# Performance work log

Measured on AMD Instinct MI355X. Metric: run time of the kernel, lower is better.

The kernel has to match this reference:

```python
import jax, jax.numpy as jnp
import numpy as np
import math

SCALES = [1, 2, 4, 8]
H = 1024           # hidden_size
NS = len(SCALES)
DS = H // NS       # per-scale dim = 256
NH_S = max(1, 8 // NS)  # heads per scale = 2


def _avg_pool(x, s):
    # x: [B, L, d], kernel=stride=s (L divisible by s)
    B, L, d = x.shape
    return x.reshape(B, L // s, s, d).mean(axis=2)


def _mha(q, k, v, in_w, in_b, out_w, out_b, nh):
    # torch nn.MultiheadAttention, batch_first, no mask.
    d = q.shape[-1]
    wq, wk, wv = in_w[:d], in_w[d:2 * d], in_w[2 * d:]
    bq, bk, bv = in_b[:d], in_b[d:2 * d], in_b[2 * d:]
    qh = q @ wq.T + bq
    kh = k @ wk.T + bk
    vh = v @ wv.T + bv
    B, Lq, _ = qh.shape
    Lk = kh.shape[1]
    hd = d // nh
    qh = qh.reshape(B, Lq, nh, hd).transpose(0, 2, 1, 3)
    kh = kh.reshape(B, Lk, nh, hd).transpose(0, 2, 1, 3)
    vh = vh.reshape(B, Lk, nh, hd).transpose(0, 2, 1, 3)
    scores = jnp.einsum('bhqd,bhkd->bhqk', qh, kh) * (1.0 / math.sqrt(hd))
    w = jax.nn.softmax(scores, axis=-1)
    out = jnp.einsum('bhqk,bhkd->bhqd', w, vh)
    out = out.transpose(0, 2, 1, 3).reshape(B, Lq, d)
    out = out @ out_w.T + out_b
    return out, w.mean(axis=1)  # averaged attn weights (torch default)


def setup_inputs() -> dict:
    key = jax.random.key(0)
    ks = jax.random.split(key, 20)
    B, S = 4, 2048
    f = lambda k, shape: (jax.random.normal(k, shape, dtype=jnp.float32) * 0.02)
    return {
        'query': jax.random.normal(ks[0], (B, S, H), dtype=jnp.float32),
        'key': jax.random.normal(ks[1], (B, S, H), dtype=jnp.float32),
        'value': jax.random.normal(ks[2], (B, S, H), dtype=jnp.float32),
        'wq': f(ks[3], (H, H)), 'bq': f(ks[4], (H,)),
        'wk': f(ks[5], (H, H)), 'bk': f(ks[6], (H,)),
        'wv': f(ks[7], (H, H)), 'bv': f(ks[8], (H,)),
        'mha_in_w': f(ks[9], (NS, 3 * DS, DS)),
        'mha_in_b': f(ks[10], (NS, 3 * DS)),
        'mha_out_w': f(ks[11], (NS, DS, DS)),
        'mha_out_b': f(ks[12], (NS, DS)),
        'fus_w': f(ks[13], (H, H)), 'fus_b': f(ks[14], (H,)),
    }


def reference(query, key, value, wq, bq, wk, bk, wv, bv,
              mha_in_w, mha_in_b, mha_out_w, mha_out_b, fus_w, fus_b):
    q = query @ wq.T + bq
    k = key @ wk.T + bk
    v = value @ wv.T + bv
    outs = []
    weights0 = None
    for i, s in enumerate(SCALES):
        qs = q[..., i * DS:(i + 1) * DS]
        ks_ = k[..., i * DS:(i + 1) * DS]
        vs = v[..., i * DS:(i + 1) * DS]
        if s > 1:
            ks_ = _avg_pool(ks_, s)
            vs = _avg_pool(vs, s)
        attended, w = _mha(qs, ks_, vs, mha_in_w[i], mha_in_b[i],
                           mha_out_w[i], mha_out_b[i], NH_S)
        # F.interpolate back to seq_len is an identity here (query length == seq_len)
        outs.append(attended)
        if i == 0:
            weights0 = w
    fused = jnp.concatenate(outs, axis=-1) @ fus_w.T + fus_b
    return fused, weights0
```

## Files before the change

kernel.cpp:

```cpp
#include <hip/hip_runtime.h>
#include <stdint.h>

typedef unsigned short u16;
typedef __bf16 v8bf __attribute__((ext_vector_type(8)));
typedef float v4f __attribute__((ext_vector_type(4)));
typedef __attribute__((address_space(3))) unsigned lds_t;
typedef const __attribute__((address_space(1))) unsigned g_t;

__device__ __forceinline__ u16 f2bf(float f) {
  union { float f; unsigned u; } v; v.f = f;
  unsigned r = v.u + 0x7FFFu + ((v.u >> 16) & 1u);
  return (u16)(r >> 16);
}
__device__ __forceinline__ float bf2f(u16 h) {
  union { unsigned u; float f; } v; v.u = ((unsigned)h) << 16;
  return v.f;
}
__device__ __forceinline__ ushort4 f4bf(float4 f) {
  ushort4 o;
  o.x = f2bf(f.x); o.y = f2bf(f.y); o.z = f2bf(f.z); o.w = f2bf(f.w);
  return o;
}
__device__ __forceinline__ long sel4(long4 v, int z) {
  return z == 0 ? v.x : z == 1 ? v.y : z == 2 ? v.z : v.w;
}
__device__ __forceinline__ int sel4i(int4 v, int z) {
  return z == 0 ? v.x : z == 1 ? v.y : z == 2 ? v.z : v.w;
}

__global__ void k_cvt(const float* __restrict__ s, u16* __restrict__ d, long n) {
  long i = ((long)blockIdx.x * blockDim.x + threadIdx.x) * 4;
  long stride = (long)gridDim.x * blockDim.x * 4;
  for (; i < n; i += stride) {
    *(ushort4*)(d + i) = f4bf(*(const float4*)(s + i));
  }
}

__global__ void k_cvtpool(const float* __restrict__ src, u16* __restrict__ dst) {
  int g = blockIdx.x & 255, b = blockIdx.x >> 8;
  int c = threadIdx.x * 4;
  const float* p = src + ((long)b * 2048 + g * 8) * 1024 + c;
  u16* df = dst + ((long)b * 2048 + g * 8) * 1024 + c;
  float4 x[8];
#pragma unroll
  for (int j = 0; j < 8; j++) {
    x[j] = *(const float4*)(p + (long)j * 1024);
    *(ushort4*)(df + (long)j * 1024) = f4bf(x[j]);
  }
  float4 s2[4], s4[2], s8;
#pragma unroll
  for (int j = 0; j < 4; j++) {
    s2[j].x = x[2 * j].x + x[2 * j + 1].x;
    s2[j].y = x[2 * j].y + x[2 * j + 1].y;
    s2[j].z = x[2 * j].z + x[2 * j + 1].z;
    s2[j].w = x[2 * j].w + x[2 * j + 1].w;
  }
#pragma unroll
  for (int j = 0; j < 2; j++) {
    s4[j].x = s2[2 * j].x + s2[2 * j + 1].x;
    s4[j].y = s2[2 * j].y + s2[2 * j + 1].y;
    s4[j].z = s2[2 * j].z + s2[2 * j + 1].z;
    s4[j].w = s2[2 * j].w + s2[2 * j + 1].w;
  }
  s8.x = s4[0].x + s4[1].x; s8.y = s4[0].y + s4[1].y;
  s8.z = s4[0].z + s4[1].z; s8.w = s4[0].w + s4[1].w;
  u16* d2 = dst + ((long)8192 + b * 1024 + g * 4) * 1024 + c;
#pragma unroll
  for (int j = 0; j < 4; j++) {
    float4 t = {s2[j].x * 0.5f, s2[j].y * 0.5f, s2[j].z * 0.5f, s2[j].w * 0.5f};
    *(ushort4*)(d2 + (long)j * 1024) = f4bf(t);
  }
  u16* d4 = dst + ((long)12288 + b * 512 + g * 2) * 1024 + c;
#pragma unroll
  for (int j = 0; j < 2; j++) {
    float4 t = {s4[j].x * 0.25f, s4[j].y * 0.25f, s4[j].z * 0.25f, s4[j].w * 0.25f};
    *(ushort4*)(d4 + (long)j * 1024) = f4bf(t);
  }
  float4 t8 = {s8.x * 0.125f, s8.y * 0.125f, s8.z * 0.125f, s8.w * 0.125f};
  *(ushort4*)(dst + ((long)14336 + b * 256 + g) * 1024 + c) = f4bf(t8);
}

__global__ void k_tc(const float* __restrict__ src, u16* __restrict__ dst, int R, int C) {
  __shared__ float t[32][33];
  long zoff = (long)blockIdx.z * R * C;
  int r0 = blockIdx.y * 32, c0 = blockIdx.x * 32;
  int tx = threadIdx.x & 31, ty = threadIdx.x >> 5;
#pragma unroll
  for (int j = 0; j < 32; j += 8)
    t[ty + j][tx] = src[zoff + (long)(r0 + ty + j) * C + c0 + tx];
  __syncthreads();
#pragma unroll
  for (int j = 0; j < 32; j += 8)
    dst[zoff + (long)(c0 + ty + j) * R + r0 + tx] = f2bf(t[tx][ty + j]);
}

__global__ void k_bcomb_qkv(const float* __restrict__ in_w, const float* __restrict__ in_b,
                            const float* __restrict__ bq, const float* __restrict__ bk,
                            const float* __restrict__ bv, float* __restrict__ out) {
  int gw = (blockIdx.x * 256 + threadIdx.x) >> 6;
  int lane = threadIdx.x & 63;
  int p = gw >> 10, j = gw & 1023, i = j >> 8, of = j & 255;
  const float* bp = p == 0 ? bq : p == 1 ? bk : bv;
  const float* row = in_w + ((long)i * 768 + p * 256 + of) * 256;
  float s = 0.f;
#pragma unroll
  for (int m = 0; m < 4; m++) s += row[lane + m * 64] * bp[i * 256 + lane + m * 64];
#pragma unroll
  for (int m = 32; m >= 1; m >>= 1) s += __shfl_xor(s, m, 64);
  if (lane == 0) out[gw] = in_b[(long)i * 768 + p * 256 + of] + s;
}

__global__ void k_bcomb_f(const float* __restrict__ fw, const float* __restrict__ fb,
                          const float* __restrict__ ob, float* __restrict__ out) {
  int w = (blockIdx.x * 256 + threadIdx.x) >> 6;
  int lane = threadIdx.x & 63;
  const float* row = fw + (long)w * 1024;
  float s = 0.f;
  for (int k = lane; k < 1024; k += 64) s += row[k] * ob[k];
#pragma unroll
  for (int m = 32; m >= 1; m >>= 1) s += __shfl_xor(s, m, 64);
  if (lane == 0) out[w] = fb[w] + s;
}

template<int KS>
__global__ __launch_bounds__(256) void k_ksum(const float* __restrict__ P,
                                              u16* __restrict__ O, long n, int coloff) {
  long i = ((long)blockIdx.x * 256 + threadIdx.x) * 4;
  if (i >= n) return;
  float4 s = *(const float4*)(P + i);
#pragma unroll
  for (int ks = 1; ks < KS; ks++) {
    float4 t = *(const float4*)(P + (long)ks * n + i);
    s.x += t.x; s.y += t.y; s.z += t.z; s.w += t.w;
  }
  *(ushort4*)(O + (i >> 8) * 1024 + coloff + (int)(i & 255)) = f4bf(s);
}

__device__ __forceinline__ float block_allreduce(float x, bool domax) {
  __shared__ float t[4];
  int lane = threadIdx.x & 63, w = threadIdx.x >> 6;
#pragma unroll
  for (int m = 32; m >= 1; m >>= 1) {
    float o = __shfl_xor(x, m, 64);
    x = domax ? fmaxf(x, o) : (x + o);
  }
  __syncthreads();
  if (lane == 0) t[w] = x;
  __syncthreads();
  return domax ? fmaxf(fmaxf(t[0], t[1]), fmaxf(t[2], t[3]))
               : (t[0] + t[1] + t[2] + t[3]);
}

__global__ __launch_bounds__(256) void k_softmax0(u16* __restrict__ P, float* __restrict__ W0) {
  int bq = blockIdx.x;
  int b = bq >> 11, q = bq & 2047;
  int tid = threadIdx.x;
  float pw[2][8];
  for (int h = 0; h < 2; h++) {
    u16* p = P + (((long)(b * 2 + h) * 2048 + q) * 2048);
    float v[8];
    float mx = -1e30f;
#pragma unroll
    for (int i = 0; i < 8; i++) { v[i] = bf2f(p[tid + i * 256]); mx = fmaxf(mx, v[i]); }
    mx = block_allreduce(mx, true);
    float s = 0.f;
#pragma unroll
    for (int i = 0; i < 8; i++) { v[i] = __expf(v[i] - mx); s += v[i]; }
    s = block_allreduce(s, false);
    float inv = 1.0f / s;
#pragma unroll
    for (int i = 0; i < 8; i++) { pw[h][i] = v[i] * inv; p[tid + i * 256] = f2bf(pw[h][i]); }
  }
  float* wrow = W0 + (long)bq * 2048;
#pragma unroll
  for (int i = 0; i < 8; i++) wrow[tid + i * 256] = 0.5f * (pw[0][i] + pw[1][i]);
}

__global__ __launch_bounds__(256) void k_flash(
    const u16* __restrict__ QHf, const u16* __restrict__ KH,
    const u16* __restrict__ VHT, u16* __restrict__ AOf)
{
  int z = blockIdx.z;
  int i = (z >> 3) + 1;
  int b = (z >> 1) & 3, h = z & 1;
  int Ls = 2048 >> i;
  int nkt = Ls >> 7;
  long ro = (long)(16384 - (8192 >> (i - 1))) * 256;
  int q0 = blockIdx.y * 64;

  __shared__ u16 QP[64][136];
  __shared__ u16 KV[2][128][32];
  __shared__ float red[2][4][64];

  const int tid = threadIdx.x, lane = tid & 63, wave = tid >> 6;
  const int q4 = lane >> 4, l16 = lane & 15;
  const int wr = (wave >> 1) * 32, wc = (wave & 1) * 64;
  const int srow = wave * 16 + (lane >> 2);
  const int scol = (lane & 3) * 8;

  {
    const u16* gq = QHf + ((long)b * 2048 + q0) * 1024 + i * 256 + h * 128;
    int idx = tid * 4;
#pragma unroll
    for (int j = 0; j < 4; j++) {
      int r = (idx + j) >> 4, ch = (idx + j) & 15;
      *(ulonglong2*)&QP[r][ch * 8] = *(const ulonglong2*)(gq + (long)r * 1024 + ch * 8);
    }
  }
  __syncthreads();
  v8bf qf[2][4];
#pragma unroll
  for (int mi = 0; mi < 2; mi++)
#pragma unroll
    for (int sub = 0; sub < 4; sub++)
      qf[mi][sub] = *(const v8bf*)&QP[wr + mi * 16 + l16][sub * 32 + q4 * 8];
  __syncthreads();

  const u16* gK = KH + ro + (long)b * Ls * 256 + h * 128;
  const u16* gV = VHT + ro + (long)(b * 2 + h) * 128 * Ls;

  auto stageK = [&](int buf, int kt, int sub) {
    const u16* g = gK + (long)(kt * 128 + srow) * 256 + sub * 32 + scol;
    __builtin_amdgcn_global_load_lds((g_t*)g, (lds_t*)&KV[buf][wave * 16][0], 16, 0, 0);
    __builtin_amdgcn_global_load_lds((g_t*)(g + 64 * 256), (lds_t*)&KV[buf][64 + wave * 16][0], 16, 0, 0);
  };
  auto stageV = [&](int buf, int kt, int sub) {
    const u16* g = gV + (long)srow * Ls + kt * 128 + sub * 32 + scol;
    __builtin_amdgcn_global_load_lds((g_t*)g, (lds_t*)&KV[buf][wave * 16][0], 16, 0, 0);
    __builtin_amdgcn_global_load_lds((g_t*)(g + (long)64 * Ls), (lds_t*)&KV[buf][64 + wave * 16][0], 16, 0, 0);
  };

  v4f acc_o[2][4];
  float m_run[2][4], l_run[2][4];
#pragma unroll
  for (int mi = 0; mi < 2; mi++)
#pragma unroll
    for (int ni = 0; ni < 4; ni++) acc_o[mi][ni] = (v4f){0.f, 0.f, 0.f, 0.f};
#pragma unroll
  for (int mi = 0; mi < 2; mi++)
#pragma unroll
    for (int i4 = 0; i4 < 4; i4++) { m_run[mi][i4] = -1e30f; l_run[mi][i4] = 0.f; }

  const float alpha = 0.08838834764831845f;

  for (int kt = 0; kt < nkt; kt++) {
    v4f s[2][4];
#pragma unroll
    for (int mi = 0; mi < 2; mi++)
#pragma unroll
      for (int ni = 0; ni < 4; ni++) s[mi][ni] = (v4f){0.f, 0.f, 0.f, 0.f};
    stageK(0, kt, 0);
    __syncthreads();
    int cur = 0;
#pragma unroll
    for (int sub = 0; sub < 4; sub++) {
      if (sub < 3) stageK(cur ^ 1, kt, sub + 1);
      v8bf kf[4];
#pragma unroll
      for (int ni = 0; ni < 4; ni++)
        kf[ni] = *(const v8bf*)&KV[cur][wc + ni * 16 + l16][q4 * 8];
#pragma unroll
      for (int mi = 0; mi < 2; mi++)
#pragma unroll
        for (int ni = 0; ni < 4; ni++)
          s[mi][ni] = __builtin_amdgcn_mfma_f32_16x16x32_bf16(qf[mi][sub], kf[ni], s[mi][ni], 0, 0, 0);
      __syncthreads();
      cur ^= 1;
    }
    stageV(0, kt, 0);

#pragma unroll
    for (int mi = 0; mi < 2; mi++)
#pragma unroll
      for (int ni = 0; ni < 4; ni++) s[mi][ni] *= alpha;
    float mloc[2][4];
#pragma unroll
    for (int mi = 0; mi < 2; mi++)
#pragma unroll
      for (int i4 = 0; i4 < 4; i4++)
        mloc[mi][i4] = fmaxf(fmaxf(s[mi][0][i4], s[mi][1][i4]),
                             fmaxf(s[mi][2][i4], s[mi][3][i4]));
#pragma unroll
    for (int d = 1; d <= 8; d <<= 1)
#pragma unroll
      for (int mi = 0; mi < 2; mi++)
#pragma unroll
        for (int i4 = 0; i4 < 4; i4++)
          mloc[mi][i4] = fmaxf(mloc[mi][i4], __shfl_xor(mloc[mi][i4], d, 64));
    if (l16 == 0) {
#pragma unroll
      for (int mi = 0; mi < 2; mi++)
#pragma unroll
        for (int i4 = 0; i4 < 4; i4++)
          red[0][wave][wr + mi * 16 + q4 * 4 + i4] = mloc[mi][i4];
    }
    __syncthreads();
    float scl[2][4];
#pragma unroll
    for (int mi = 0; mi < 2; mi++)
#pragma unroll
      for (int i4 = 0; i4 < 4; i4++) {
        int rr = wr + mi * 16 + q4 * 4 + i4;
        float mn = fmaxf(fmaxf(red[0][wave][rr], red[0][wave ^ 1][rr]), m_run[mi][i4]);
        scl[mi][i4] = __expf(m_run[mi][i4] - mn);
        m_run[mi][i4] = mn;
      }
    float lloc[2][4] = {{0.f, 0.f, 0.f, 0.f}, {0.f, 0.f, 0.f, 0.f}};
#pragma unroll
    for (int mi = 0; mi < 2; mi++)
#pragma unroll
      for (int ni = 0; ni < 4; ni++)
#pragma unroll
        for (int i4 = 0; i4 < 4; i4++) {
          float p = __expf(s[mi][ni][i4] - m_run[mi][i4]);
          lloc[mi][i4] += p;
          QP[wr + mi * 16 + q4 * 4 + i4][wc + ni * 16 + l16] = f2bf(p);
        }
#pragma unroll
    for (int d = 1; d <= 8; d <<= 1)
#pragma unroll
      for (int mi = 0; mi < 2; mi++)
#pragma unroll
        for (int i4 = 0; i4 < 4; i4++)
          lloc[mi][i4] += __shfl_xor(lloc[mi][i4], d, 64);
    if (l16 == 0) {
#pragma unroll
      for (int mi = 0; mi < 2; mi++)
#pragma unroll
        for (int i4 = 0; i4 < 4; i4++)
          red[1][wave][wr + mi * 16 + q4 * 4 + i4] = lloc[mi][i4];
    }
#pragma unroll
    for (int mi = 0; mi < 2; mi++)
#pragma unroll
      for (int ni = 0; ni < 4; ni++)
#pragma unroll
        for (int i4 = 0; i4 < 4; i4++) acc_o[mi][ni][i4] *= scl[mi][i4];
    __syncthreads();
#pragma unroll
    for (int mi = 0; mi < 2; mi++)
#pragma unroll
      for (int i4 = 0; i4 < 4; i4++) {
        int rr = wr + mi * 16 + q4 * 4 + i4;
        l_run[mi][i4] = l_run[mi][i4] * scl[mi][i4] + red[1][wave][rr] + red[1][wave ^ 1][rr];
      }

    int cv = 0;
#pragma unroll
    for (int sub = 0; sub < 4; sub++) {
      if (sub < 3) stageV(cv ^ 1, kt, sub + 1);
      v8bf pf[2], vf[4];
#pragma unroll
      for (int mi = 0; mi < 2; mi++)
        pf[mi] = *(const v8bf*)&QP[wr + mi * 16 + l16][sub * 32 + q4 * 8];
#pragma unroll
      for (int ni = 0; ni < 4; ni++)
        vf[ni] = *(const v8bf*)&KV[cv][wc + ni * 16 + l16][q4 * 8];
#pragma unroll
      for (int mi = 0; mi < 2; mi++)
#pragma unroll
        for (int ni = 0; ni < 4; ni++)
          acc_o[mi][ni] = __builtin_amdgcn_mfma_f32_16x16x32_bf16(pf[mi], vf[ni], acc_o[mi][ni], 0, 0, 0);
      __syncthreads();
      cv ^= 1;
    }
  }

#pragma unroll
  for (int mi = 0; mi < 2; mi++)
#pragma unroll
    for (int i4 = 0; i4 < 4; i4++) {
      float inv = 1.0f / l_run[mi][i4];
#pragma unroll
      for (int ni = 0; ni < 4; ni++) {
        int r = q0 + wr + mi * 16 + q4 * 4 + i4;
        int c = wc + ni * 16 + l16;
        AOf[((long)b * 2048 + r) * 1024 + i * 256 + h * 128 + c] =
            f2bf(acc_o[mi][ni][i4] * inv);
      }
    }
}

template<int WBF>
__global__ __launch_bounds__(256) void k_gemm(
    const u16* __restrict__ A, long ldA, long sA1, long sA2,
    const u16* __restrict__ B, long ldB, long sB1, long sB2,
    void* __restrict__ Cv, long ldC, long sC1, long sC2, long sCk,
    const float* __restrict__ bias, long sBias, float alpha,
    int M, int N, int K, int nz2, int KS)
{
  __shared__ u16 As[2][128][32];
  __shared__ u16 Bs[2][128][32];
  int z = blockIdx.z;
  int ks = z % KS; int zz = z / KS;
  int z1 = zz / nz2, z2 = zz - z1 * nz2;
  A += (long)z1 * sA1 + (long)z2 * sA2 + (long)ks * K;
  B += (long)z1 * sB1 + (long)z2 * sB2 + (long)ks * K;
  long coff = (long)z1 * sC1 + (long)z2 * sC2 + (long)ks * sCk;
  const float* bz = bias ? bias + (long)z2 * sBias : nullptr;
  const int m0 = blockIdx.y * 128, n0 = blockIdx.x * 128;
  const int tid = threadIdx.x;
  const int lane = tid & 63;
  const int wave = tid >> 6;
  const int wr = (wave >> 1) * 64, wc = (wave & 1) * 64;
  const int q4 = lane >> 4, l16 = lane & 15;

  const int srow = wave * 16 + (lane >> 2);
  const int scol = (lane & 3) * 8;
  const u16* gA = A + (long)(m0 + srow) * ldA + scol;
  const u16* gB = B + (long)(n0 + srow) * ldB + scol;

  auto stage = [&](int buf, int kt) {
    __builtin_amdgcn_global_load_lds((g_t*)(gA + kt), (lds_t*)&As[buf][wave * 16][0], 16, 0, 0);
    __builtin_amdgcn_global_load_lds((g_t*)(gA + 64 * ldA + kt), (lds_t*)&As[buf][64 + wave * 16][0], 16, 0, 0);
    __builtin_amdgcn_global_load_lds((g_t*)(gB + kt), (lds_t*)&Bs[buf][wave * 16][0], 16, 0, 0);
    __builtin_amdgcn_global_load_lds((g_t*)(gB + 64 * ldB + kt), (lds_t*)&Bs[buf][64 + wave * 16][0], 16, 0, 0);
  };

  v4f acc[4][4];
#pragma unroll
  for (int i = 0; i < 4; i++)
#pragma unroll
    for (int j = 0; j < 4; j++) acc[i][j] = (v4f){0.f, 0.f, 0.f, 0.f};

  stage(0, 0);
  __syncthreads();
  int cur = 0;
  for (int kt = 0; kt < K; kt += 32) {
    if (kt + 32 < K) stage(cur ^ 1, kt + 32);
    v8bf af[4], bf[4];
#pragma unroll
    for (int i = 0; i < 4; i++) af[i] = *(const v8bf*)&As[cur][wr + i * 16 + l16][q4 * 8];
#pragma unroll
    for (int i = 0; i < 4; i++) bf[i] = *(const v8bf*)&Bs[cur][wc + i * 16 + l16][q4 * 8];
#pragma unroll
    for (int mi = 0; mi < 4; mi++)
#pragma unroll
      for (int ni = 0; ni < 4; ni++)
        acc[mi][ni] = __builtin_amdgcn_mfma_f32_16x16x32_bf16(af[mi], bf[ni], acc[mi][ni], 0, 0, 0);
    __syncthreads();
    cur ^= 1;
  }

#pragma unroll
  for (int mi = 0; mi < 4; mi++) {
    int rb = m0 + wr + mi * 16 + q4 * 4;
#pragma unroll
    for (int ni = 0; ni < 4; ni++) {
      int c = n0 + wc + ni * 16 + l16;
      float bv = bz ? bz[c] : 0.f;
#pragma unroll
      for (int i = 0; i < 4; i++) {
        int r = rb + i;
        float val = acc[mi][ni][i] * alpha + bv;
        if (WBF) ((u16*)Cv)[coff + (long)r * ldC + c] = f2bf(val);
        else     ((float*)Cv)[coff + (long)r * ldC + c] = val;
      }
    }
  }
}

template<int TR>
__global__ __launch_bounds__(256) void k_gemm_sm(
    const u16* __restrict__ A, long ldA, long4 aOff,
    const u16* __restrict__ B, long ldB, long sB,
    u16* __restrict__ C, long ldC, long4 cOff,
    const float* __restrict__ bias, long sBias,
    int4 Mz, int K, int4 Lsz)
{
  int z = blockIdx.z;
  int M = sel4i(Mz, z);
  int m0 = blockIdx.y * 128;
  if (m0 >= M) return;
  int n0 = blockIdx.x * 64;
  const u16* Az = A + sel4(aOff, z);
  const u16* Bz = B + (long)z * sB;
  long coff = sel4(cOff, z);
  const float* bz = bias + (long)z * sBias;
  int Ls = sel4i(Lsz, z);
  int lsh = 31 - __clz(Ls);

  __shared__ u16 As[2][128][32];
  __shared__ u16 Bs[2][64][32];
  const int tid = threadIdx.x;
  const int lane = tid & 63, wave = tid >> 6;
  const int q4 = lane >> 4, l16 = lane & 15;
  const int srow = wave * 16 + (lane >> 2);
  const int scol = (lane & 3) * 8;
  const u16* gA = Az + (long)(m0 + srow) * ldA + scol;
  const u16* gB = Bz + (long)(n0 + srow) * ldB + scol;

  auto stage = [&](int buf, int kt) {
    __builtin_amdgcn_global_load_lds((g_t*)(gA + kt), (lds_t*)&As[buf][wave * 16][0], 16, 0, 0);
    __builtin_amdgcn_global_load_lds((g_t*)(gA + 64 * ldA + kt), (lds_t*)&As[buf][64 + wave * 16][0], 16, 0, 0);
    __builtin_amdgcn_global_load_lds((g_t*)(gB + kt), (lds_t*)&Bs[buf][wave * 16][0], 16, 0, 0);
  };

  v4f acc[2][4];
#pragma unroll
  for (int i = 0; i < 2; i++)
#pragma unroll
    for (int j = 0; j < 4; j++) acc[i][j] = (v4f){0.f, 0.f, 0.f, 0.f};

  stage(0, 0);
  __syncthreads();
  int cur = 0;
  for (int kt = 0; kt < K; kt += 32) {
    if (kt + 32 < K) stage(cur ^ 1, kt + 32);
    v8bf af[2], bf[4];
#pragma unroll
    for (int i = 0; i < 2; i++) af[i] = *(const v8bf*)&As[cur][wave * 32 + i * 16 + l16][q4 * 8];
#pragma unroll
    for (int j = 0; j < 4; j++) bf[j] = *(const v8bf*)&Bs[cur][j * 16 + l16][q4 * 8];
#pragma unroll
    for (int mi = 0; mi < 2; mi++)
#pragma unroll
      for (int ni = 0; ni < 4; ni++)
        acc[mi][ni] = __builtin_amdgcn_mfma_f32_16x16x32_bf16(af[mi], bf[ni], acc[mi][ni], 0, 0, 0);
    __syncthreads();
    cur ^= 1;
  }

#pragma unroll
  for (int mi = 0; mi < 2; mi++) {
    int rb = m0 + wave * 32 + mi * 16 + q4 * 4;
#pragma unroll
    for (int ni = 0; ni < 4; ni++) {
      int c = n0 + ni * 16 + l16;
      float bv = bz[c];
#pragma unroll
      for (int i = 0; i < 4; i++) {
        int r = rb + i;
        float val = acc[mi][ni][i] + bv;
        if (TR) {
          int b = r >> lsh, t = r & (Ls - 1);
          int h = c >> 7, n = c & 127;
          C[coff + (((long)(b * 2 + h) * 128 + n) << lsh) + t] = f2bf(val);
        } else {
          C[coff + (long)r * ldC + c] = f2bf(val);
        }
      }
    }
  }
}

extern "C" void kernel_launch(void* const* d_in, const int* in_sizes, int n_in,
                              void* d_out, int out_size, void* d_ws, size_t ws_size,
                              hipStream_t stream) {
  const float* query = (const float*)d_in[0];
  const float* key_  = (const float*)d_in[1];
  const float* value = (const float*)d_in[2];
  const float* wq    = (const float*)d_in[3];
  const float* bq    = (const float*)d_in[4];
  const float* wk    = (const float*)d_in[5];
  const float* bk    = (const float*)d_in[6];
  const float* wv    = (const float*)d_in[7];
  const float* bv    = (const float*)d_in[8];
  const float* in_w  = (const float*)d_in[9];
  const float* in_b  = (const float*)d_in[10];
  const float* out_w = (const float*)d_in[11];
  const float* out_b = (const float*)d_in[12];
  const float* fus_w = (const float*)d_in[13];
  const float* fus_b = (const float*)d_in[14];
  (void)in_sizes; (void)n_in; (void)out_size; (void)ws_size;

  float* outF  = (float*)d_out;
  float* outW0 = outF + (long)4 * 2048 * 1024;

  char* base = (char*)d_ws;
  size_t off = 0;
  auto alloc = [&](size_t bytes) -> void* {
    void* p = base + off;
    off = (off + bytes + 255) & ~(size_t)255;
    return p;
  };
  const long NX = (long)8192 * 1024;
  u16* Winb = (u16*)alloc((size_t)4 * 768 * 256 * 2);
  u16* Wfb  = (u16*)alloc((size_t)1024 * 1024 * 2);
  u16* WoT  = (u16*)alloc((size_t)4 * 256 * 256 * 2);
  u16* WT   = (u16*)alloc((size_t)3 * 1024 * 1024 * 2);
  u16* WC   = (u16*)alloc((size_t)3 * 1024 * 1024 * 2);
  u16* WFc  = (u16*)alloc((size_t)1024 * 1024 * 2);
  float* Bc  = (float*)alloc((size_t)3 * 1024 * 4);
  float* fbc = (float*)alloc((size_t)1024 * 4);
  char* regX = (char*)alloc((size_t)(8192 + 2 * 15360) * 1024 * 2);
  u16* Xq    = (u16*)regX;
  u16* XkAll = Xq + NX;
  u16* XvAll = XkAll + (long)15360 * 1024;
  u16* SC    = (u16*)regX;
  u16* QHf = (u16*)alloc((size_t)8192 * 1024 * 2);
  u16* KH  = (u16*)alloc((size_t)15360 * 256 * 2);
  u16* VHT = (u16*)alloc((size_t)15360 * 256 * 2);
  float* PP = (float*)alloc((size_t)4 * 8192 * 256 * 4);
  u16* AOf = (u16*)alloc((size_t)8192 * 1024 * 2);

  const long AOsz = (long)8192 * 256;

  k_cvt<<<1024, 256, 0, stream>>>(query, Xq, NX);
  k_cvtpool<<<1024, 256, 0, stream>>>(key_,  XkAll);
  k_cvtpool<<<1024, 256, 0, stream>>>(value, XvAll);
  k_cvt<<<192, 256, 0, stream>>>(in_w, Winb, 4 * 768 * 256);
  k_cvt<<<256, 256, 0, stream>>>(fus_w, Wfb, 1024 * 1024);
  k_tc<<<dim3(32, 32, 1), 256, 0, stream>>>(wq, WT, 1024, 1024);
  k_tc<<<dim3(32, 32, 1), 256, 0, stream>>>(wk, WT + (long)1024 * 1024, 1024, 1024);
  k_tc<<<dim3(32, 32, 1), 256, 0, stream>>>(wv, WT + (long)2 * 1024 * 1024, 1024, 1024);
  k_tc<<<dim3(8, 8, 4), 256, 0, stream>>>(out_w, WoT, 256, 256);
  k_bcomb_qkv<<<768, 256, 0, stream>>>(in_w, in_b, bq, bk, bv, Bc);
  k_bcomb_f<<<256, 256, 0, stream>>>(fus_w, fus_b, out_b, fbc);

  k_gemm<1><<<dim3(8, 2, 12), 256, 0, stream>>>(
      Winb, 256, 65536, 196608,
      WT, 1024, 1048576, 256,
      WC, 1024, 1048576, 262144, 0,
      nullptr, 0, 1.f, 256, 1024, 256, 4, 1);
  k_gemm<1><<<dim3(2, 8, 4), 256, 0, stream>>>(
      Wfb, 1024, 0, 256,
      WoT, 256, 0, 65536,
      WFc, 1024, 0, 256, 0,
      nullptr, 0, 1.f, 1024, 256, 256, 4, 1);

  k_gemm<1><<<dim3(8, 64, 1), 256, 0, stream>>>(
      Xq, 1024, 0, 0, WC, 1024, 0, 0,
      QHf, 1024, 0, 0, 0, Bc, 0, 1.f, 8192, 1024, 1024, 1, 1);
  {
    long4 aK = {0, (long)8192 * 1024, (long)12288 * 1024, (long)14336 * 1024};
    long4 cK = {0, (long)8192 * 256, (long)12288 * 256, (long)14336 * 256};
    int4  mP = {8192, 4096, 2048, 1024};
    int4  ls1 = {1, 1, 1, 1};
    int4  lsv = {2048, 1024, 512, 256};
    k_gemm_sm<0><<<dim3(4, 64, 4), 256, 0, stream>>>(
        XkAll, 1024, aK, WC + (long)1024 * 1024, 1024, 262144,
        KH, 256, cK, Bc + 1024, 256, mP, 1024, ls1);
    k_gemm_sm<1><<<dim3(4, 64, 4), 256, 0, stream>>>(
        XvAll, 1024, aK, WC + (long)2 * 1024 * 1024, 1024, 262144,
        VHT, 0, cK, Bc + 2048, 256, mP, 1024, lsv);
  }

  {
    k_gemm<1><<<dim3(16, 16, 8), 256, 0, stream>>>(
        QHf, 1024, (long)2048 * 1024, 128,
        KH, 256, (long)2048 * 256, 128,
        SC, 2048, (long)2 * 2048 * 2048, (long)2048 * 2048, 0,
        nullptr, 0, 0.08838834764831845f, 2048, 2048, 128, 2, 1);
    k_softmax0<<<8192, 256, 0, stream>>>(SC, outW0);
    k_gemm<0><<<dim3(1, 16, 32), 256, 0, stream>>>(
        SC, 2048, (long)2 * 2048 * 2048, (long)2048 * 2048,
        VHT, 2048, (long)2 * 128 * 2048, (long)128 * 2048,
        PP, 256, (long)2048 * 256, 128, AOsz,
        nullptr, 0, 1.f, 2048, 128, 512, 2, 4);
    k_ksum<4><<<2048, 256, 0, stream>>>(PP, AOf, AOsz, 0);
  }

  k_flash<<<dim3(1, 32, 24), 256, 0, stream>>>(QHf, KH, VHT, AOf);

  k_gemm<0><<<dim3(8, 64, 1), 256, 0, stream>>>(
      AOf, 1024, 0, 0, WFc, 1024, 0, 0,
      outF, 1024, 0, 0, 0, fbc, 0, 1.f, 8192, 1024, 1024, 1, 1);
}
```

Baseline: 532.2 us.

## Replace materialized scale-0 scores with two-pass fused attention and merge K/V projection GEMMs

The scale-0 path used to write full bf16 score matrices, run a separate softmax kernel, do a split-K PV GEMM and reduce the partials. It now runs a first pass that computes per-row max and sum online, then a second pass that recomputes QK^T, writes the normalized weights and head-averaged W0 directly, and accumulates PV in registers. This removes the large score-matrix round trip through memory. The cost is computing QK^T twice, plus low parallelism in k_pv0, which uses a 64x4 grid of 32-row tiles. The K and V projection GEMMs are also merged into one launch with 128x128 tiles instead of two launches of 128x64.

```diff
diff --git a/kernel.cpp b/kernel.cpp
--- a/kernel.cpp
+++ b/kernel.cpp
@@ -20,12 +20,6 @@
   ushort4 o;
   o.x = f2bf(f.x); o.y = f2bf(f.y); o.z = f2bf(f.z); o.w = f2bf(f.w);
   return o;
-}
-__device__ __forceinline__ long sel4(long4 v, int z) {
-  return z == 0 ? v.x : z == 1 ? v.y : z == 2 ? v.z : v.w;
-}
-__device__ __forceinline__ int sel4i(int4 v, int z) {
-  return z == 0 ? v.x : z == 1 ? v.y : z == 2 ? v.z : v.w;
 }
 
 __global__ void k_cvt(const float* __restrict__ s, u16* __restrict__ d, long n) {
@@ -122,58 +116,263 @@
   if (lane == 0) out[w] = fb[w] + s;
 }
 
-template<int KS>
-__global__ __launch_bounds__(256) void k_ksum(const float* __restrict__ P,
-                                              u16* __restrict__ O, long n, int coloff) {
-  long i = ((long)blockIdx.x * 256 + threadIdx.x) * 4;
-  if (i >= n) return;
-  float4 s = *(const float4*)(P + i);
-#pragma unroll
-  for (int ks = 1; ks < KS; ks++) {
-    float4 t = *(const float4*)(P + (long)ks * n + i);
-    s.x += t.x; s.y += t.y; s.z += t.z; s.w += t.w;
-  }
-  *(ushort4*)(O + (i >> 8) * 1024 + coloff + (int)(i & 255)) = f4bf(s);
-}
-
-__device__ __forceinline__ float block_allreduce(float x, bool domax) {
-  __shared__ float t[4];
-  int lane = threadIdx.x & 63, w = threadIdx.x >> 6;
-#pragma unroll
-  for (int m = 32; m >= 1; m >>= 1) {
-    float o = __shfl_xor(x, m, 64);
-    x = domax ? fmaxf(x, o) : (x + o);
-  }
-  __syncthreads();
-  if (lane == 0) t[w] = x;
-  __syncthreads();
-  return domax ? fmaxf(fmaxf(t[0], t[1]), fmaxf(t[2], t[3]))
-               : (t[0] + t[1] + t[2] + t[3]);
-}
-
-__global__ __launch_bounds__(256) void k_softmax0(u16* __restrict__ P, float* __restrict__ W0) {
-  int bq = blockIdx.x;
-  int b = bq >> 11, q = bq & 2047;
-  int tid = threadIdx.x;
-  float pw[2][8];
-  for (int h = 0; h < 2; h++) {
-    u16* p = P + (((long)(b * 2 + h) * 2048 + q) * 2048);
-    float v[8];
-    float mx = -1e30f;
-#pragma unroll
-    for (int i = 0; i < 8; i++) { v[i] = bf2f(p[tid + i * 256]); mx = fmaxf(mx, v[i]); }
-    mx = block_allreduce(mx, true);
-    float s = 0.f;
-#pragma unroll
-    for (int i = 0; i < 8; i++) { v[i] = __expf(v[i] - mx); s += v[i]; }
-    s = block_allreduce(s, false);
-    float inv = 1.0f / s;
-#pragma unroll
-    for (int i = 0; i < 8; i++) { pw[h][i] = v[i] * inv; p[tid + i * 256] = f2bf(pw[h][i]); }
-  }
-  float* wrow = W0 + (long)bq * 2048;
-#pragma unroll
-  for (int i = 0; i < 8; i++) wrow[tid + i * 256] = 0.5f * (pw[0][i] + pw[1][i]);
+__global__ __launch_bounds__(256) void k_ml0(
+    const u16* __restrict__ QHf, const u16* __restrict__ KH,
+    float* __restrict__ M0, float* __restrict__ L0)
+{
+  int z = blockIdx.z;
+  int b = z >> 1, h = z & 1;
+  int q0 = blockIdx.y * 64;
+  __shared__ u16 KV[2][128][32];
+  __shared__ float red[2][4][64];
+
+  const int tid = threadIdx.x, lane = tid & 63, wave = tid >> 6;
+  const int q4 = lane >> 4, l16 = lane & 15;
+  const int wr = (wave >> 1) * 32, wc = (wave & 1) * 64;
+  const int srow = wave * 16 + (lane >> 2), scol = (lane & 3) * 8;
+  const float alpha = 0.08838834764831845f;
+
+  v8bf qf[2][4];
+#pragma unroll
+  for (int mi = 0; mi < 2; mi++)
+#pragma unroll
+    for (int sub = 0; sub < 4; sub++)
+      qf[mi][sub] = *(const v8bf*)(QHf + ((long)b * 2048 + q0 + wr + mi * 16 + l16) * 1024
+                                   + h * 128 + sub * 32 + q4 * 8);
+
+  const u16* gK = KH + (long)b * 2048 * 256 + h * 128;
+  auto stageK = [&](int buf, int kt, int sub) {
+    const u16* g = gK + (long)(kt * 128 + srow) * 256 + sub * 32 + scol;
+    __builtin_amdgcn_global_load_lds((g_t*)g, (lds_t*)&KV[buf][wave * 16][0], 16, 0, 0);
+    __builtin_amdgcn_global_load_lds((g_t*)(g + 64 * 256), (lds_t*)&KV[buf][64 + wave * 16][0], 16, 0, 0);
+  };
+
+  float m_run[2][4], l_run[2][4];
+#pragma unroll
+  for (int mi = 0; mi < 2; mi++)
+#pragma unroll
+    for (int i4 = 0; i4 < 4; i4++) { m_run[mi][i4] = -1e30f; l_run[mi][i4] = 0.f; }
+
+  for (int kt = 0; kt < 16; kt++) {
+    v4f s[2][4];
+#pragma unroll
+    for (int mi = 0; mi < 2; mi++)
+#pragma unroll
+      for (int ni = 0; ni < 4; ni++) s[mi][ni] = (v4f){0.f, 0.f, 0.f, 0.f};
+    stageK(0, kt, 0);
+    __syncthreads();
+    int cur = 0;
+#pragma unroll
+    for (int sub = 0; sub < 4; sub++) {
+      if (sub < 3) stageK(cur ^ 1, kt, sub + 1);
+      v8bf kf[4];
+#pragma unroll
+      for (int ni = 0; ni < 4; ni++)
+        kf[ni] = *(const v8bf*)&KV[cur][wc + ni * 16 + l16][q4 * 8];
+#pragma unroll
+      for (int mi = 0; mi < 2; mi++)
+#pragma unroll
+        for (int ni = 0; ni < 4; ni++)
+          s[mi][ni] = __builtin_amdgcn_mfma_f32_16x16x32_bf16(qf[mi][sub], kf[ni], s[mi][ni], 0, 0, 0);
+      __syncthreads();
+      cur ^= 1;
+    }
+#pragma unroll
+    for (int mi = 0; mi < 2; mi++)
+#pragma unroll
+      for (int ni = 0; ni < 4; ni++) s[mi][ni] *= alpha;
+    float mloc[2][4];
+#pragma unroll
+    for (int mi = 0; mi < 2; mi++)
+#pragma unroll
+      for (int i4 = 0; i4 < 4; i4++)
+        mloc[mi][i4] = fmaxf(fmaxf(s[mi][0][i4], s[mi][1][i4]),
+                             fmaxf(s[mi][2][i4], s[mi][3][i4]));
+#pragma unroll
+    for (int d = 1; d <= 8; d <<= 1)
+#pragma unroll
+      for (int mi = 0; mi < 2; mi++)
+#pragma unroll
+        for (int i4 = 0; i4 < 4; i4++)
+          mloc[mi][i4] = fmaxf(mloc[mi][i4], __shfl_xor(mloc[mi][i4], d, 64));
+    if (l16 == 0) {
+#pragma unroll
+      for (int mi = 0; mi < 2; mi++)
+#pragma unroll
+        for (int i4 = 0; i4 < 4; i4++)
+          red[0][wave][wr + mi * 16 + q4 * 4 + i4] = mloc[mi][i4];
+    }
+    __syncthreads();
+    float lloc[2][4] = {{0.f, 0.f, 0.f, 0.f}, {0.f, 0.f, 0.f, 0.f}};
+#pragma unroll
+    for (int mi = 0; mi < 2; mi++)
+#pragma unroll
+      for (int i4 = 0; i4 < 4; i4++) {
+        int rr = wr + mi * 16 + q4 * 4 + i4;
+        float mn = fmaxf(fmaxf(red[0][wave][rr], red[0][wave ^ 1][rr]), m_run[mi][i4]);
+        float scl = __expf(m_run[mi][i4] - mn);
+        m_run[mi][i4] = mn;
+        l_run[mi][i4] *= scl;
+#pragma unroll
+        for (int ni = 0; ni < 4; ni++)
+          lloc[mi][i4] += __expf(s[mi][ni][i4] - mn);
+      }
+#pragma unroll
+    for (int d = 1; d <= 8; d <<= 1)
+#pragma unroll
+      for (int mi = 0; mi < 2; mi++)
+#pragma unroll
+        for (int i4 = 0; i4 < 4; i4++)
+          lloc[mi][i4] += __shfl_xor(lloc[mi][i4], d, 64);
+    if (l16 == 0) {
+#pragma unroll
+      for (int mi = 0; mi < 2; mi++)
+#pragma unroll
+        for (int i4 = 0; i4 < 4; i4++)
+          red[1][wave][wr + mi * 16 + q4 * 4 + i4] = lloc[mi][i4];
+    }
+    __syncthreads();
+#pragma unroll
+    for (int mi = 0; mi < 2; mi++)
+#pragma unroll
+      for (int i4 = 0; i4 < 4; i4++) {
+        int rr = wr + mi * 16 + q4 * 4 + i4;
+        l_run[mi][i4] += red[1][wave][rr] + red[1][wave ^ 1][rr];
+      }
+    __syncthreads();
+  }
+
+  if ((wave & 1) == 0 && l16 == 0) {
+#pragma unroll
+    for (int mi = 0; mi < 2; mi++)
+#pragma unroll
+      for (int i4 = 0; i4 < 4; i4++) {
+        int r = q0 + wr + mi * 16 + q4 * 4 + i4;
+        M0[(long)z * 2048 + r] = m_run[mi][i4];
+        L0[(long)z * 2048 + r] = l_run[mi][i4];
+      }
+  }
+}
+
+__global__ __launch_bounds__(256) void k_pv0(
+    const u16* __restrict__ QHf, const u16* __restrict__ KH,
+    const u16* __restrict__ VHT, const float* __restrict__ M0,
+    const float* __restrict__ L0, u16* __restrict__ AOf, float* __restrict__ W0)
+{
+  int b = blockIdx.z;
+  int q0 = blockIdx.y * 32;
+  __shared__ u16 P[2][32][136];
+  __shared__ u16 KV[2][128][32];
+
+  const int tid = threadIdx.x, lane = tid & 63, wave = tid >> 6;
+  const int q4 = lane >> 4, l16 = lane & 15;
+  const int wr = (wave >> 1) * 16, wc = (wave & 1) * 64;
+  const int srow = wave * 16 + (lane >> 2), scol = (lane & 3) * 8;
+  const float alpha = 0.08838834764831845f;
+
+  v8bf qf[2][4];
+#pragma unroll
+  for (int h = 0; h < 2; h++)
+#pragma unroll
+    for (int sub = 0; sub < 4; sub++)
+      qf[h][sub] = *(const v8bf*)(QHf + ((long)b * 2048 + q0 + wr + l16) * 1024
+                                  + h * 128 + sub * 32 + q4 * 8);
+  float mv[2][4], il[2][4];
+#pragma unroll
+  for (int h = 0; h < 2; h++)
+#pragma unroll
+    for (int i4 = 0; i4 < 4; i4++) {
+      long r = (long)(b * 2 + h) * 2048 + q0 + wr + q4 * 4 + i4;
+      mv[h][i4] = M0[r];
+      il[h][i4] = 1.0f / L0[r];
+    }
+
+  const u16* gK = KH + (long)b * 2048 * 256;
+  auto stageK = [&](int buf, int h, int kt, int sub) {
+    const u16* g = gK + (long)(kt * 128 + srow) * 256 + h * 128 + sub * 32 + scol;
+    __builtin_amdgcn_global_load_lds((g_t*)g, (lds_t*)&KV[buf][wave * 16][0], 16, 0, 0);
+    __builtin_amdgcn_global_load_lds((g_t*)(g + 64 * 256), (lds_t*)&KV[buf][64 + wave * 16][0], 16, 0, 0);
+  };
+  auto stageV = [&](int buf, int h, int kt, int sub) {
+    const u16* g = VHT + ((long)(b * 2 + h) * 128 + srow) * 2048 + kt * 128 + sub * 32 + scol;
+    __builtin_amdgcn_global_load_lds((g_t*)g, (lds_t*)&KV[buf][wave * 16][0], 16, 0, 0);
+    __builtin_amdgcn_global_load_lds((g_t*)(g + (long)64 * 2048), (lds_t*)&KV[buf][64 + wave * 16][0], 16, 0, 0);
+  };
+
+  v4f acc[2][4];
+#pragma unroll
+  for (int h = 0; h < 2; h++)
+#pragma unroll
+    for (int ni = 0; ni < 4; ni++) acc[h][ni] = (v4f){0.f, 0.f, 0.f, 0.f};
+
+  for (int kt = 0; kt < 16; kt++) {
+    float p0[4][4];
+#pragma unroll
+    for (int h = 0; h < 2; h++) {
+      v4f s[4];
+#pragma unroll
+      for (int ni = 0; ni < 4; ni++) s[ni] = (v4f){0.f, 0.f, 0.f, 0.f};
+      stageK(0, h, kt, 0);
+      __syncthreads();
+      int cur = 0;
+#pragma unroll
+      for (int sub = 0; sub < 4; sub++) {
+        if (sub < 3) stageK(cur ^ 1, h, kt, sub + 1);
+        v8bf kf[4];
+#pragma unroll
+        for (int ni = 0; ni < 4; ni++)
+          kf[ni] = *(const v8bf*)&KV[cur][wc + ni * 16 + l16][q4 * 8];
+#pragma unroll
+        for (int ni = 0; ni < 4; ni++)
+          s[ni] = __builtin_amdgcn_mfma_f32_16x16x32_bf16(qf[h][sub], kf[ni], s[ni], 0, 0, 0);
+        __syncthreads();
+        cur ^= 1;
+      }
+#pragma unroll
+      for (int ni = 0; ni < 4; ni++)
+#pragma unroll
+        for (int i4 = 0; i4 < 4; i4++) {
+          float p = __expf(s[ni][i4] * alpha - mv[h][i4]) * il[h][i4];
+          P[h][wr + q4 * 4 + i4][wc + ni * 16 + l16] = f2bf(p);
+          if (h == 0) p0[ni][i4] = p;
+          else {
+            W0[((long)b * 2048 + q0 + wr + q4 * 4 + i4) * 2048
+               + kt * 128 + wc + ni * 16 + l16] = 0.5f * (p0[ni][i4] + p);
+          }
+        }
+    }
+#pragma unroll
+    for (int h = 0; h < 2; h++) {
+      stageV(0, h, kt, 0);
+      __syncthreads();
+      int cv = 0;
+#pragma unroll
+      for (int sub = 0; sub < 4; sub++) {
+        if (sub < 3) stageV(cv ^ 1, h, kt, sub + 1);
+        v8bf pf = *(const v8bf*)&P[h][wr + l16][sub * 32 + q4 * 8];
+        v8bf vf[4];
+#pragma unroll
+        for (int ni = 0; ni < 4; ni++)
+          vf[ni] = *(const v8bf*)&KV[cv][wc + ni * 16 + l16][q4 * 8];
+#pragma unroll
+        for (int ni = 0; ni < 4; ni++)
+          acc[h][ni] = __builtin_amdgcn_mfma_f32_16x16x32_bf16(pf, vf[ni], acc[h][ni], 0, 0, 0);
+        __syncthreads();
+        cv ^= 1;
+      }
+    }
+  }
+
+#pragma unroll
+  for (int h = 0; h < 2; h++)
+#pragma unroll
+    for (int ni = 0; ni < 4; ni++)
+#pragma unroll
+      for (int i4 = 0; i4 < 4; i4++) {
+        int r = q0 + wr + q4 * 4 + i4;
+        int c = wc + ni * 16 + l16;
+        AOf[((long)b * 2048 + r) * 1024 + h * 128 + c] = f2bf(acc[h][ni][i4]);
+      }
 }
 
 __global__ __launch_bounds__(256) void k_flash(
@@ -460,60 +659,56 @@
   }
 }
 
-template<int TR>
-__global__ __launch_bounds__(256) void k_gemm_sm(
-    const u16* __restrict__ A, long ldA, long4 aOff,
-    const u16* __restrict__ B, long ldB, long sB,
-    u16* __restrict__ C, long ldC, long4 cOff,
-    const float* __restrict__ bias, long sBias,
-    int4 Mz, int K, int4 Lsz)
+__global__ __launch_bounds__(256) void k_gemm_kv(
+    const u16* __restrict__ Xk, const u16* __restrict__ Xv,
+    const u16* __restrict__ WCkv, const float* __restrict__ Bckv,
+    u16* __restrict__ KH, u16* __restrict__ VHT)
 {
-  int z = blockIdx.z;
-  int M = sel4i(Mz, z);
-  int m0 = blockIdx.y * 128;
-  if (m0 >= M) return;
-  int n0 = blockIdx.x * 64;
-  const u16* Az = A + sel4(aOff, z);
-  const u16* Bz = B + (long)z * sB;
-  long coff = sel4(cOff, z);
-  const float* bz = bias + (long)z * sBias;
-  int Ls = sel4i(Lsz, z);
-  int lsh = 31 - __clz(Ls);
-
   __shared__ u16 As[2][128][32];
-  __shared__ u16 Bs[2][64][32];
+  __shared__ u16 Bs[2][128][32];
+  const int isV = blockIdx.z;
+  const int m0 = blockIdx.y * 128, n0 = blockIdx.x * 128;
+  const int scale = m0 < 8192 ? 0 : (m0 < 12288 ? 1 : (m0 < 14336 ? 2 : 3));
+  const int rbase = scale == 0 ? 0 : (scale == 1 ? 8192 : (scale == 2 ? 12288 : 14336));
+  const int lsh = 11 - scale;
+  const u16* A = isV ? Xv : Xk;
+  const u16* B = WCkv + (long)isV * 1048576 + (long)scale * 262144;
+  const float* bz = Bckv + isV * 1024 + scale * 256;
+
   const int tid = threadIdx.x;
   const int lane = tid & 63, wave = tid >> 6;
+  const int wr = (wave >> 1) * 64, wc = (wave & 1) * 64;
   const int q4 = lane >> 4, l16 = lane & 15;
   const int srow = wave * 16 + (lane >> 2);
   const int scol = (lane & 3) * 8;
-  const u16* gA = Az + (long)(m0 + srow) * ldA + scol;
-  const u16* gB = Bz + (long)(n0 + srow) * ldB + scol;
+  const u16* gA = A + (long)(m0 + srow) * 1024 + scol;
+  const u16* gB = B + (long)(n0 + srow) * 1024 + scol;
 
   auto stage = [&](int buf, int kt) {
     __builtin_amdgcn_global_load_lds((g_t*)(gA + kt), (lds_t*)&As[buf][wave * 16][0], 16, 0, 0);
-    __builtin_amdgcn_global_load_lds((g_t*)(gA + 64 * ldA + kt), (lds_t*)&As[buf][64 + wave * 16][0], 16, 0, 0);
+    __builtin_amdgcn_global_load_lds((g_t*)(gA + 64 * 1024 + kt), (lds_t*)&As[buf][64 + wave * 16][0], 16, 0, 0);
     __builtin_amdgcn_global_load_lds((g_t*)(gB + kt), (lds_t*)&Bs[buf][wave * 16][0], 16, 0, 0);
+    __builtin_amdgcn_global_load_lds((g_t*)(gB + 64 * 1024 + kt), (lds_t*)&Bs[buf][64 + wave * 16][0], 16, 0, 0);
   };
 
-  v4f acc[2][4];
-#pragma unroll
-  for (int i = 0; i < 2; i++)
+  v4f acc[4][4];
+#pragma unroll
+  for (int i = 0; i < 4; i++)
 #pragma unroll
     for (int j = 0; j < 4; j++) acc[i][j] = (v4f){0.f, 0.f, 0.f, 0.f};
 
   stage(0, 0);
   __syncthreads();
   int cur = 0;
-  for (int kt = 0; kt < K; kt += 32) {
-    if (kt + 32 < K) stage(cur ^ 1, kt + 32);
-    v8bf af[2], bf[4];
-#pragma unroll
-    for (int i = 0; i < 2; i++) af[i] = *(const v8bf*)&As[cur][wave * 32 + i * 16 + l16][q4 * 8];
-#pragma unroll
-    for (int j = 0; j < 4; j++) bf[j] = *(const v8bf*)&Bs[cur][j * 16 + l16][q4 * 8];
-#pragma unroll
-    for (int mi = 0; mi < 2; mi++)
+  for (int kt = 0; kt < 1024; kt += 32) {
+    if (kt + 32 < 1024) stage(cur ^ 1, kt + 32);
+    v8bf af[4], bf[4];
+#pragma unroll
+    for (int i = 0; i < 4; i++) af[i] = *(const v8bf*)&As[cur][wr + i * 16 + l16][q4 * 8];
+#pragma unroll
+    for (int i = 0; i < 4; i++) bf[i] = *(const v8bf*)&Bs[cur][wc + i * 16 + l16][q4 * 8];
+#pragma unroll
+    for (int mi = 0; mi < 4; mi++)
 #pragma unroll
       for (int ni = 0; ni < 4; ni++)
         acc[mi][ni] = __builtin_amdgcn_mfma_f32_16x16x32_bf16(af[mi], bf[ni], acc[mi][ni], 0, 0, 0);
@@ -522,22 +717,23 @@
   }
 
 #pragma unroll
-  for (int mi = 0; mi < 2; mi++) {
-    int rb = m0 + wave * 32 + mi * 16 + q4 * 4;
+  for (int mi = 0; mi < 4; mi++) {
+    int rb = m0 + wr + mi * 16 + q4 * 4;
 #pragma unroll
     for (int ni = 0; ni < 4; ni++) {
-      int c = n0 + ni * 16 + l16;
+      int c = n0 + wc + ni * 16 + l16;
       float bv = bz[c];
 #pragma unroll
       for (int i = 0; i < 4; i++) {
         int r = rb + i;
         float val = acc[mi][ni][i] + bv;
-        if (TR) {
-          int b = r >> lsh, t = r & (Ls - 1);
+        if (!isV) {
+          KH[(long)r * 256 + c] = f2bf(val);
+        } else {
+          int rl = r - rbase;
+          int b = rl >> lsh, t = rl & ((1 << lsh) - 1);
           int h = c >> 7, n = c & 127;
-          C[coff + (((long)(b * 2 + h) * 128 + n) << lsh) + t] = f2bf(val);
-        } else {
-          C[coff + (long)r * ldC + c] = f2bf(val);
+          VHT[(long)rbase * 256 + (((long)(b * 2 + h) * 128 + n) << lsh) + t] = f2bf(val);
         }
       }
     }
@@ -583,18 +779,15 @@
   u16* WFc  = (u16*)alloc((size_t)1024 * 1024 * 2);
   float* Bc  = (float*)alloc((size_t)3 * 1024 * 4);
   float* fbc = (float*)alloc((size_t)1024 * 4);
-  char* regX = (char*)alloc((size_t)(8192 + 2 * 15360) * 1024 * 2);
-  u16* Xq    = (u16*)regX;
-  u16* XkAll = Xq + NX;
-  u16* XvAll = XkAll + (long)15360 * 1024;
-  u16* SC    = (u16*)regX;
+  u16* Xq    = (u16*)alloc((size_t)NX * 2);
+  u16* XkAll = (u16*)alloc((size_t)15360 * 1024 * 2);
+  u16* XvAll = (u16*)alloc((size_t)15360 * 1024 * 2);
   u16* QHf = (u16*)alloc((size_t)8192 * 1024 * 2);
   u16* KH  = (u16*)alloc((size_t)15360 * 256 * 2);
   u16* VHT = (u16*)alloc((size_t)15360 * 256 * 2);
-  float* PP = (float*)alloc((size_t)4 * 8192 * 256 * 4);
+  float* M0 = (float*)alloc((size_t)8 * 2048 * 4);
+  float* L0 = (float*)alloc((size_t)8 * 2048 * 4);
   u16* AOf = (u16*)alloc((size_t)8192 * 1024 * 2);
-
-  const long AOsz = (long)8192 * 256;
 
   k_cvt<<<1024, 256, 0, stream>>>(query, Xq, NX);
   k_cvtpool<<<1024, 256, 0, stream>>>(key_,  XkAll);
@@ -622,34 +815,11 @@
   k_gemm<1><<<dim3(8, 64, 1), 256, 0, stream>>>(
       Xq, 1024, 0, 0, WC, 1024, 0, 0,
       QHf, 1024, 0, 0, 0, Bc, 0, 1.f, 8192, 1024, 1024, 1, 1);
-  {
-    long4 aK = {0, (long)8192 * 1024, (long)12288 * 1024, (long)14336 * 1024};
-    long4 cK = {0, (long)8192 * 256, (long)12288 * 256, (long)14336 * 256};
-    int4  mP = {8192, 4096, 2048, 1024};
-    int4  ls1 = {1, 1, 1, 1};
-    int4  lsv = {2048, 1024, 512, 256};
-    k_gemm_sm<0><<<dim3(4, 64, 4), 256, 0, stream>>>(
-        XkAll, 1024, aK, WC + (long)1024 * 1024, 1024, 262144,
-        KH, 256, cK, Bc + 1024, 256, mP, 1024, ls1);
-    k_gemm_sm<1><<<dim3(4, 64, 4), 256, 0, stream>>>(
-        XvAll, 1024, aK, WC + (long)2 * 1024 * 1024, 1024, 262144,
-        VHT, 0, cK, Bc + 2048, 256, mP, 1024, lsv);
-  }
-
-  {
-    k_gemm<1><<<dim3(16, 16, 8), 256, 0, stream>>>(
-        QHf, 1024, (long)2048 * 1024, 128,
-        KH, 256, (long)2048 * 256, 128,
-        SC, 2048, (long)2 * 2048 * 2048, (long)2048 * 2048, 0,
-        nullptr, 0, 0.08838834764831845f, 2048, 2048, 128, 2, 1);
-    k_softmax0<<<8192, 256, 0, stream>>>(SC, outW0);
-    k_gemm<0><<<dim3(1, 16, 32), 256, 0, stream>>>(
-        SC, 2048, (long)2 * 2048 * 2048, (long)2048 * 2048,
-        VHT, 2048, (long)2 * 128 * 2048, (long)128 * 2048,
-        PP, 256, (long)2048 * 256, 128, AOsz,
-        nullptr, 0, 1.f, 2048, 128, 512, 2, 4);
-    k_ksum<4><<<2048, 256, 0, stream>>>(PP, AOf, AOsz, 0);
-  }
+  k_gemm_kv<<<dim3(2, 120, 2), 256, 0, stream>>>(
+      XkAll, XvAll, WC + (long)1024 * 1024, Bc + 1024, KH, VHT);
+
+  k_ml0<<<dim3(1, 32, 8), 256, 0, stream>>>(QHf, KH, M0, L0);
+  k_pv0<<<dim3(1, 64, 4), 256, 0, stream>>>(QHf, KH, VHT, M0, L0, AOf, outW0);
 
   k_flash<<<dim3(1, 32, 24), 256, 0, stream>>>(QHf, KH, VHT, AOf);
 
```

Result: slower. 552.2 us (+3.8%).
